# Optimization experiments

Measured on AMD Instinct MI355X. Metric: run time of the kernel, lower is better.

The kernel has to match this reference:

```python
import jax, jax.numpy as jnp
import numpy as np

B, C_IN, H, W_SP = 16, 128, 56, 56
C_OUT, KH, KW = 256, 3, 3
STRIDE = (1, 1)
PADDING = (1, 1)


def setup_inputs() -> dict:
    key = jax.random.key(0)
    kx, kw = jax.random.split(key)
    x = jax.random.normal(kx, (B, C_IN, H, W_SP), dtype=jnp.float32)
    W = jax.random.normal(kw, (C_OUT, C_IN, KH, KW), dtype=jnp.float32) * 0.01
    b = jnp.zeros((C_OUT,), dtype=jnp.float32)
    return {"x": x, "W": W, "b": b}


def reference(x, W, b):
    # NCHW direct convolution, same math as the nested-loop torch module.
    out = jax.lax.conv_general_dilated(
        x, W,
        window_strides=STRIDE,
        padding=[(PADDING[0], PADDING[0]), (PADDING[1], PADDING[1])],
        dimension_numbers=("NCHW", "OIHW", "NCHW"),
    )
    return out + b[None, :, None, None]
```

## Files before the change

kernel.cpp:

```cpp
#include <hip/hip_runtime.h>

typedef __attribute__((ext_vector_type(8))) short short8;
typedef __attribute__((ext_vector_type(4))) float f32x4;

#define CI    128
#define CO_   256
#define HW_   56
#define PLANE 3136
#define NB    16
#define STOT  50176
#define KTOT  1152
#define OUTN  802816

#define XT_BYTES   12845056ull
#define WP_USHORTS 294912
#define WS_NEED    (12845056ull + 589824ull + 256ull)

__device__ __forceinline__ unsigned short f2bf(float f) {
  unsigned u = __float_as_uint(f);
  u += 0x7FFFu + ((u >> 16) & 1u);
  return (unsigned short)(u >> 16);
}

__device__ __forceinline__ void gload16(void* lds, const void* g) {
  __builtin_amdgcn_global_load_lds(
      (const __attribute__((address_space(1))) unsigned int*)g,
      (__attribute__((address_space(3))) unsigned int*)lds, 16, 0, 0);
}

template <int N> __device__ __forceinline__ void vmwait() {
  asm volatile("s_waitcnt vmcnt(%0)" ::"n"(N) : "memory");
}

__global__ __launch_bounds__(256) void prep_x(const float* __restrict__ X,
                                              unsigned short* __restrict__ Xt) {
  __shared__ __align__(16) unsigned short tile[32][132];
  const int t = threadIdx.x;
  const int bx = blockIdx.x;
  const int n   = bx / 100;
  const int rem = bx % 100;
  const int cib = rem / 25;
  const int spb = rem % 25;
  const int sp0 = spb * 128;
  const float* src = X + (size_t)(n * CI + cib * 32) * PLANE;
#pragma unroll
  for (int j = 0; j < 4; ++j) {
    int f = t + 256 * j;
    int ci  = f >> 5;
    int sp4 = (f & 31) * 4;
    if (sp0 + sp4 < PLANE) {
      f32x4 v = *(const f32x4*)(src + (size_t)ci * PLANE + sp0 + sp4);
#pragma unroll
      for (int e = 0; e < 4; ++e) tile[ci][sp4 + e] = f2bf(v[e]);
    }
  }
  __syncthreads();
  unsigned short* dst = Xt + ((size_t)n * PLANE + sp0) * CI + cib * 32;
#pragma unroll
  for (int j = 0; j < 2; ++j) {
    int g = t + 256 * j;
    int sp = g >> 2;
    int q  = g & 3;
    if (sp0 + sp < PLANE) {
      short8 v;
#pragma unroll
      for (int e = 0; e < 8; ++e) v[e] = (short)tile[q * 8 + e][sp];
      *(short8*)(dst + (size_t)sp * CI + q * 8) = v;
    }
  }
}

__global__ __launch_bounds__(256) void prep_w(const float* __restrict__ W,
                                              unsigned short* __restrict__ Wp) {
  const int u = blockIdx.x * 256 + threadIdx.x;
  const int rcbmt = u >> 9;
  const int p     = u & 511;
  const int mt  = rcbmt & 1;
  const int rcb = rcbmt >> 1;
  const int cb  = rcb & 3;
  const int r   = rcb >> 2;
  const int col = p >> 2;
  const int kg  = (p & 3) ^ ((col >> 1) & 3);
  const int co  = mt * 128 + col;
  const int ci0 = cb * 32 + kg * 8;
  short8 v;
#pragma unroll
  for (int e = 0; e < 8; ++e)
    v[e] = (short)f2bf(W[(size_t)co * KTOT + (size_t)(ci0 + e) * 9 + r]);
  *(short8*)(Wp + (size_t)u * 8) = v;
  if (u < 16) {
    short8 z = {0, 0, 0, 0, 0, 0, 0, 0};
    *(short8*)(Wp + WP_USHORTS + u * 8) = z;
  }
}

__global__ __launch_bounds__(256) void conv_gemm(const unsigned short* __restrict__ Xt,
                                                 const unsigned short* __restrict__ Wp,
                                                 const float* __restrict__ bias,
                                                 float* __restrict__ out) {
  __shared__ __align__(1024) char smem[49152];
  const int t    = threadIdx.x;
  const int lane = t & 63;
  const int wid  = t >> 6;
  const int wm   = wid >> 1, wn = wid & 1;

  int bx = blockIdx.x;
  bx = (bx & 7) * 98 + (bx >> 3);
  const int mt  = bx & 1;
  const int spt = bx >> 1;

  const int kgB = (t & 3) ^ ((t >> 3) & 3);
  const int S0 = spt * 128 + (t >> 2);
  const int S1 = S0 + 64;
  const int hw0 = S0 % PLANE, h0 = hw0 / HW_, w0 = hw0 - h0 * HW_;
  const int hw1 = S1 % PLANE, h1 = hw1 / HW_, w1 = hw1 - h1 * HW_;

  const char* xb0  = (const char*)Xt + ((size_t)S0 * CI + kgB * 8) * 2;
  const char* xb1  = (const char*)Xt + ((size_t)S1 * CI + kgB * 8) * 2;
  const char* zb   = (const char*)(Wp + WP_USHORTS) + kgB * 16;
  const char* wpA  = (const char*)Wp + mt * 8192 + t * 16;

  const int swz  = ((lane >> 4) ^ ((lane >> 1) & 3)) * 16;
  const int aoff = (wm * 64 + (lane & 15)) * 64 + swz;
  const int boff = 8192 + (wn * 64 + (lane & 15)) * 64 + swz;

  f32x4 acc[4][4];
  const f32x4 zf = {0.f, 0.f, 0.f, 0.f};
#pragma unroll
  for (int m = 0; m < 4; ++m)
#pragma unroll
    for (int n = 0; n < 4; ++n) acc[m][n] = zf;

  auto STAGE = [&](int s) {
    const int r_  = (s >> 2) , cb_ = s & 3;
    const int dh_ = r_ / 3 - 1, dw_ = r_ % 3 - 1;
    const int ro_ = dh_ * HW_ + dw_;
    char* dst = smem + (s % 3) * 16384 + wid * 1024;
    const char* as = wpA + r_ * 65536 + cb_ * 16384;
    gload16(dst, as);
    gload16(dst + 4096, as + 4096);
    const bool v0 = ((unsigned)(h0 + dh_) < HW_) & ((unsigned)(w0 + dw_) < HW_);
    const bool v1 = ((unsigned)(h1 + dh_) < HW_) & ((unsigned)(w1 + dw_) < HW_);
    const char* b0 = v0 ? xb0 + ro_ * 256 + cb_ * 64 : zb + cb_ * 64;
    const char* b1 = v1 ? xb1 + ro_ * 256 + cb_ * 64 : zb + cb_ * 64;
    gload16(dst + 8192, b0);
    gload16(dst + 12288, b1);
  };

  STAGE(0);
  STAGE(1);
  STAGE(2);

#pragma unroll
  for (int s = 0; s < 36; ++s) {
    if (s <= 33)      vmwait<8>();
    else if (s == 34) vmwait<4>();
    else              vmwait<0>();
    __builtin_amdgcn_s_barrier();

    const char* rb = smem + (s % 3) * 16384;
    short8 a[4], b[4];
#pragma unroll
    for (int m = 0; m < 4; ++m) a[m] = *(const short8*)(rb + aoff + m * 1024);
#pragma unroll
    for (int n = 0; n < 4; ++n) b[n] = *(const short8*)(rb + boff + n * 1024);
#pragma unroll
    for (int m = 0; m < 4; ++m)
#pragma unroll
      for (int n = 0; n < 4; ++n)
        acc[m][n] = __builtin_amdgcn_mfma_f32_16x16x32_bf16(a[m], b[n], acc[m][n], 0, 0, 0);

    if (s < 33) {
      __builtin_amdgcn_s_barrier();
      STAGE(s + 3);
    }
  }

  float bv[4][4];
#pragma unroll
  for (int mf = 0; mf < 4; ++mf) {
    int cobase = mt * 128 + wm * 64 + mf * 16 + (lane >> 4) * 4;
#pragma unroll
    for (int r2 = 0; r2 < 4; ++r2) bv[mf][r2] = bias[cobase + r2];
  }
#pragma unroll
  for (int nf = 0; nf < 4; ++nf) {
    int S = spt * 128 + wn * 64 + nf * 16 + (lane & 15);
    int n = S / PLANE, hw = S - n * PLANE;
    float* ob = out + (size_t)n * OUTN + hw;
#pragma unroll
    for (int mf = 0; mf < 4; ++mf) {
      int cobase = mt * 128 + wm * 64 + mf * 16 + (lane >> 4) * 4;
#pragma unroll
      for (int r2 = 0; r2 < 4; ++r2)
        ob[(size_t)(cobase + r2) * PLANE] = acc[mf][nf][r2] + bv[mf][r2];
    }
  }
}

__global__ __launch_bounds__(256) void conv_naive(const float* __restrict__ X,
                                                  const float* __restrict__ W,
                                                  const float* __restrict__ bias,
                                                  float* __restrict__ out) {
  int idx = blockIdx.x * 256 + threadIdx.x;
  int hw = idx % PLANE;
  int co = (idx / PLANE) & 255;
  int n  = idx / (PLANE * 256);
  int h = hw / HW_, w = hw - h * HW_;
  float acc = bias[co];
  const float* xp = X + (size_t)n * CI * PLANE;
  const float* wp = W + (size_t)co * KTOT;
  for (int ci = 0; ci < CI; ++ci) {
#pragma unroll
    for (int kh = 0; kh < 3; ++kh) {
      int y = h + kh - 1;
      if ((unsigned)y >= HW_) continue;
#pragma unroll
      for (int kw = 0; kw < 3; ++kw) {
        int x = w + kw - 1;
        if ((unsigned)x >= HW_) continue;
        acc += xp[(size_t)ci * PLANE + y * HW_ + x] * wp[ci * 9 + kh * 3 + kw];
      }
    }
  }
  out[idx] = acc;
}

extern "C" void kernel_launch(void* const* d_in, const int* in_sizes, int n_in,
                              void* d_out, int out_size, void* d_ws, size_t ws_size,
                              hipStream_t stream) {
  (void)in_sizes; (void)n_in; (void)out_size;
  const float* X = (const float*)d_in[0];
  const float* W = (const float*)d_in[1];
  const float* b = (const float*)d_in[2];
  float* out = (float*)d_out;
  if (ws_size >= WS_NEED) {
    unsigned short* Xt = (unsigned short*)d_ws;
    unsigned short* Wp = (unsigned short*)((char*)d_ws + XT_BYTES);
    prep_x<<<1600, 256, 0, stream>>>(X, Xt);
    prep_w<<<144, 256, 0, stream>>>(W, Wp);
    conv_gemm<<<784, 256, 0, stream>>>(Xt, Wp, b, out);
  } else {
    conv_naive<<<(NB * CO_ * PLANE + 255) / 256, 256, 0, stream>>>(X, W, b, out);
  }
}
```

Before: 55.09 us.

## Split Xt into per-channel-block planes, fuse prep kernels, add MFMA priority

Merges the x and weight prep kernels into one launch, saving one kernel launch. Relayouts the bf16 activation buffer into four planes of 32 channels each, so every B-tile load per stage reads a contiguous 64-byte row per spatial position. Each wave now loads its own 32-position slice. Also precomputes the 9-tap boundary masks as bitmasks, raises wave priority around the MFMA block, sets launch_bounds occupancy to 3, and reads bias directly in the epilogue. The risks are changed LDS write locality and higher register pressure under the occupancy hint.

```diff
diff --git a/kernel.cpp b/kernel.cpp
--- a/kernel.cpp
+++ b/kernel.cpp
@@ -11,6 +11,7 @@
 #define STOT  50176
 #define KTOT  1152
 #define OUTN  802816
+#define PLSZ  3211264ull
 
 #define XT_BYTES   12845056ull
 #define WP_USHORTS 294912
@@ -32,72 +33,73 @@
   asm volatile("s_waitcnt vmcnt(%0)" ::"n"(N) : "memory");
 }
 
-__global__ __launch_bounds__(256) void prep_x(const float* __restrict__ X,
-                                              unsigned short* __restrict__ Xt) {
-  __shared__ __align__(16) unsigned short tile[32][132];
+__global__ __launch_bounds__(256) void prep_fused(const float* __restrict__ X,
+                                                  const float* __restrict__ W,
+                                                  unsigned short* __restrict__ Xt,
+                                                  unsigned short* __restrict__ Wp) {
   const int t = threadIdx.x;
-  const int bx = blockIdx.x;
-  const int n   = bx / 100;
-  const int rem = bx % 100;
-  const int cib = rem / 25;
-  const int spb = rem % 25;
-  const int sp0 = spb * 128;
-  const float* src = X + (size_t)(n * CI + cib * 32) * PLANE;
-#pragma unroll
-  for (int j = 0; j < 4; ++j) {
-    int f = t + 256 * j;
-    int ci  = f >> 5;
-    int sp4 = (f & 31) * 4;
-    if (sp0 + sp4 < PLANE) {
-      f32x4 v = *(const f32x4*)(src + (size_t)ci * PLANE + sp0 + sp4);
-#pragma unroll
-      for (int e = 0; e < 4; ++e) tile[ci][sp4 + e] = f2bf(v[e]);
-    }
-  }
-  __syncthreads();
-  unsigned short* dst = Xt + ((size_t)n * PLANE + sp0) * CI + cib * 32;
-#pragma unroll
-  for (int j = 0; j < 2; ++j) {
-    int g = t + 256 * j;
-    int sp = g >> 2;
-    int q  = g & 3;
-    if (sp0 + sp < PLANE) {
-      short8 v;
-#pragma unroll
-      for (int e = 0; e < 8; ++e) v[e] = (short)tile[q * 8 + e][sp];
-      *(short8*)(dst + (size_t)sp * CI + q * 8) = v;
-    }
-  }
-}
-
-__global__ __launch_bounds__(256) void prep_w(const float* __restrict__ W,
-                                              unsigned short* __restrict__ Wp) {
-  const int u = blockIdx.x * 256 + threadIdx.x;
-  const int rcbmt = u >> 9;
-  const int p     = u & 511;
-  const int mt  = rcbmt & 1;
-  const int rcb = rcbmt >> 1;
-  const int cb  = rcb & 3;
-  const int r   = rcb >> 2;
-  const int col = p >> 2;
-  const int kg  = (p & 3) ^ ((col >> 1) & 3);
-  const int co  = mt * 128 + col;
-  const int ci0 = cb * 32 + kg * 8;
-  short8 v;
-#pragma unroll
-  for (int e = 0; e < 8; ++e)
-    v[e] = (short)f2bf(W[(size_t)co * KTOT + (size_t)(ci0 + e) * 9 + r]);
-  *(short8*)(Wp + (size_t)u * 8) = v;
-  if (u < 16) {
-    short8 z = {0, 0, 0, 0, 0, 0, 0, 0};
-    *(short8*)(Wp + WP_USHORTS + u * 8) = z;
-  }
-}
-
-__global__ __launch_bounds__(256) void conv_gemm(const unsigned short* __restrict__ Xt,
-                                                 const unsigned short* __restrict__ Wp,
-                                                 const float* __restrict__ bias,
-                                                 float* __restrict__ out) {
+  if (blockIdx.x < 1600) {
+    __shared__ __align__(16) unsigned short tile[32][132];
+    const int bx = blockIdx.x;
+    const int n   = bx / 100;
+    const int rem = bx % 100;
+    const int cib = rem / 25;
+    const int spb = rem % 25;
+    const int sp0 = spb * 128;
+    const float* src = X + (size_t)(n * CI + cib * 32) * PLANE;
+#pragma unroll
+    for (int j = 0; j < 4; ++j) {
+      int f = t + 256 * j;
+      int ci  = f >> 5;
+      int sp4 = (f & 31) * 4;
+      if (sp0 + sp4 < PLANE) {
+        f32x4 v = *(const f32x4*)(src + (size_t)ci * PLANE + sp0 + sp4);
+#pragma unroll
+        for (int e = 0; e < 4; ++e) tile[ci][sp4 + e] = f2bf(v[e]);
+      }
+    }
+    __syncthreads();
+    unsigned short* dstp = Xt + (size_t)cib * (PLSZ / 2) + ((size_t)n * PLANE + sp0) * 32;
+#pragma unroll
+    for (int j = 0; j < 2; ++j) {
+      int g = t + 256 * j;
+      int sp = g >> 2;
+      int q  = g & 3;
+      if (sp0 + sp < PLANE) {
+        short8 v;
+#pragma unroll
+        for (int e = 0; e < 8; ++e) v[e] = (short)tile[q * 8 + e][sp];
+        *(short8*)(dstp + (size_t)sp * 32 + q * 8) = v;
+      }
+    }
+  } else {
+    const int u = (blockIdx.x - 1600) * 256 + t;
+    const int rcbmt = u >> 9;
+    const int p     = u & 511;
+    const int mt  = rcbmt & 1;
+    const int rcb = rcbmt >> 1;
+    const int cb  = rcb & 3;
+    const int r   = rcb >> 2;
+    const int col = p >> 2;
+    const int kg  = (p & 3) ^ ((col >> 1) & 3);
+    const int co  = mt * 128 + col;
+    const int ci0 = cb * 32 + kg * 8;
+    short8 v;
+#pragma unroll
+    for (int e = 0; e < 8; ++e)
+      v[e] = (short)f2bf(W[(size_t)co * KTOT + (size_t)(ci0 + e) * 9 + r]);
+    *(short8*)(Wp + (size_t)u * 8) = v;
+    if (u < 16) {
+      short8 z = {0, 0, 0, 0, 0, 0, 0, 0};
+      *(short8*)(Wp + WP_USHORTS + u * 8) = z;
+    }
+  }
+}
+
+__global__ __launch_bounds__(256, 3) void conv_gemm(const unsigned short* __restrict__ Xt,
+                                                    const unsigned short* __restrict__ Wp,
+                                                    const float* __restrict__ bias,
+                                                    float* __restrict__ out) {
   __shared__ __align__(1024) char smem[49152];
   const int t    = threadIdx.x;
   const int lane = t & 63;
@@ -109,16 +111,22 @@
   const int mt  = bx & 1;
   const int spt = bx >> 1;
 
-  const int kgB = (t & 3) ^ ((t >> 3) & 3);
-  const int S0 = spt * 128 + (t >> 2);
-  const int S1 = S0 + 64;
+  const int kgB = (lane & 3) ^ ((lane >> 3) & 3);
+  const int S0 = spt * 128 + wid * 32 + (lane >> 2);
+  const int S1 = S0 + 16;
   const int hw0 = S0 % PLANE, h0 = hw0 / HW_, w0 = hw0 - h0 * HW_;
   const int hw1 = S1 % PLANE, h1 = hw1 / HW_, w1 = hw1 - h1 * HW_;
-
-  const char* xb0  = (const char*)Xt + ((size_t)S0 * CI + kgB * 8) * 2;
-  const char* xb1  = (const char*)Xt + ((size_t)S1 * CI + kgB * 8) * 2;
-  const char* zb   = (const char*)(Wp + WP_USHORTS) + kgB * 16;
-  const char* wpA  = (const char*)Wp + mt * 8192 + t * 16;
+  int vm0 = 0, vm1 = 0;
+#pragma unroll
+  for (int r = 0; r < 9; ++r) {
+    int dh = r / 3 - 1, dw = r % 3 - 1;
+    vm0 |= (int)(((unsigned)(h0 + dh) < HW_) & ((unsigned)(w0 + dw) < HW_)) << r;
+    vm1 |= (int)(((unsigned)(h1 + dh) < HW_) & ((unsigned)(w1 + dw) < HW_)) << r;
+  }
+  const char* xb0 = (const char*)Xt + (size_t)S0 * 64 + kgB * 16;
+  const char* xb1 = (const char*)Xt + (size_t)S1 * 64 + kgB * 16;
+  const char* zb  = (const char*)(Wp + WP_USHORTS) + (lane & 3) * 16;
+  const char* wpA = (const char*)Wp + mt * 8192 + t * 16;
 
   const int swz  = ((lane >> 4) ^ ((lane >> 1) & 3)) * 16;
   const int aoff = (wm * 64 + (lane & 15)) * 64 + swz;
@@ -131,25 +139,22 @@
 #pragma unroll
     for (int n = 0; n < 4; ++n) acc[m][n] = zf;
 
-  auto STAGE = [&](int s) {
-    const int r_  = (s >> 2) , cb_ = s & 3;
-    const int dh_ = r_ / 3 - 1, dw_ = r_ % 3 - 1;
-    const int ro_ = dh_ * HW_ + dw_;
-    char* dst = smem + (s % 3) * 16384 + wid * 1024;
-    const char* as = wpA + r_ * 65536 + cb_ * 16384;
-    gload16(dst, as);
-    gload16(dst + 4096, as + 4096);
-    const bool v0 = ((unsigned)(h0 + dh_) < HW_) & ((unsigned)(w0 + dw_) < HW_);
-    const bool v1 = ((unsigned)(h1 + dh_) < HW_) & ((unsigned)(w1 + dw_) < HW_);
-    const char* b0 = v0 ? xb0 + ro_ * 256 + cb_ * 64 : zb + cb_ * 64;
-    const char* b1 = v1 ? xb1 + ro_ * 256 + cb_ * 64 : zb + cb_ * 64;
-    gload16(dst + 8192, b0);
-    gload16(dst + 12288, b1);
+  auto STAGE = [&](int s1) {
+    char* buf = smem + (s1 % 3) * 16384;
+    const int r = s1 >> 2, cb = s1 & 3;
+    const int dh = r / 3 - 1, dw = r % 3 - 1;
+    const long  ro = (long)(dh * HW_ + dw) * 64 + (long)cb * PLSZ;
+    const char* as = wpA + r * 65536 + cb * 16384;
+    char* abuf = buf + wid * 1024;
+    gload16(abuf, as);
+    gload16(abuf + 4096, as + 4096);
+    const bool v0 = (vm0 >> r) & 1;
+    const bool v1 = (vm1 >> r) & 1;
+    gload16(buf + 8192 + wid * 2048,        v0 ? xb0 + ro : zb);
+    gload16(buf + 8192 + wid * 2048 + 1024, v1 ? xb1 + ro : zb);
   };
 
-  STAGE(0);
-  STAGE(1);
-  STAGE(2);
+  STAGE(0); STAGE(1); STAGE(2);
 
 #pragma unroll
   for (int s = 0; s < 36; ++s) {
@@ -164,11 +169,14 @@
     for (int m = 0; m < 4; ++m) a[m] = *(const short8*)(rb + aoff + m * 1024);
 #pragma unroll
     for (int n = 0; n < 4; ++n) b[n] = *(const short8*)(rb + boff + n * 1024);
+
+    __builtin_amdgcn_s_setprio(1);
 #pragma unroll
     for (int m = 0; m < 4; ++m)
 #pragma unroll
       for (int n = 0; n < 4; ++n)
         acc[m][n] = __builtin_amdgcn_mfma_f32_16x16x32_bf16(a[m], b[n], acc[m][n], 0, 0, 0);
+    __builtin_amdgcn_s_setprio(0);
 
     if (s < 33) {
       __builtin_amdgcn_s_barrier();
@@ -176,24 +184,17 @@
     }
   }
 
-  float bv[4][4];
-#pragma unroll
-  for (int mf = 0; mf < 4; ++mf) {
-    int cobase = mt * 128 + wm * 64 + mf * 16 + (lane >> 4) * 4;
-#pragma unroll
-    for (int r2 = 0; r2 < 4; ++r2) bv[mf][r2] = bias[cobase + r2];
-  }
 #pragma unroll
   for (int nf = 0; nf < 4; ++nf) {
     int S = spt * 128 + wn * 64 + nf * 16 + (lane & 15);
-    int n = S / PLANE, hw = S - n * PLANE;
-    float* ob = out + (size_t)n * OUTN + hw;
+    int nimg = S / PLANE, hw = S - nimg * PLANE;
+    float* ob = out + (size_t)nimg * OUTN + hw;
 #pragma unroll
     for (int mf = 0; mf < 4; ++mf) {
-      int cobase = mt * 128 + wm * 64 + mf * 16 + (lane >> 4) * 4;
+      int cob = mt * 128 + wm * 64 + mf * 16 + (lane >> 4) * 4;
 #pragma unroll
       for (int r2 = 0; r2 < 4; ++r2)
-        ob[(size_t)(cobase + r2) * PLANE] = acc[mf][nf][r2] + bv[mf][r2];
+        ob[(size_t)(cob + r2) * PLANE] = acc[mf][nf][r2] + bias[cob + r2];
     }
   }
 }
@@ -237,8 +238,7 @@
   if (ws_size >= WS_NEED) {
     unsigned short* Xt = (unsigned short*)d_ws;
     unsigned short* Wp = (unsigned short*)((char*)d_ws + XT_BYTES);
-    prep_x<<<1600, 256, 0, stream>>>(X, Xt);
-    prep_w<<<144, 256, 0, stream>>>(W, Wp);
+    prep_fused<<<1744, 256, 0, stream>>>(X, W, Xt, Wp);
     conv_gemm<<<784, 256, 0, stream>>>(Xt, Wp, b, out);
   } else {
     conv_naive<<<(NB * CO_ * PLANE + 255) / 256, 256, 0, stream>>>(X, W, b, out);
```

Measured after the change: 50.32 us, median of 2. -8.7%, faster.
